# Kernel tuning notes

Measured on AMD Instinct MI355X. Metric: run time of the kernel, lower is better.

Reference implementation:

```python
import jax, jax.numpy as jnp
import numpy as np

B, D_MODEL, HIDEEN, HEAD, IMG_H, IMG_W = 16, 512, 512, 8, 32, 32
D_K = D_MODEL // HEAD
EPS = 1e-5


def setup_inputs() -> dict:
    key = jax.random.key(0)
    ks = jax.random.split(key, 9)
    s_in = 1.0 / np.sqrt(D_MODEL)
    s_h = 1.0 / np.sqrt(HIDEEN)
    return {
        "x": jax.random.normal(ks[0], (B, D_MODEL, IMG_H, IMG_W), jnp.float32),
        "Wq": jax.random.uniform(ks[1], (HIDEEN, D_MODEL), jnp.float32, -s_in, s_in),
        "bq": jax.random.uniform(ks[2], (HIDEEN,), jnp.float32, -s_in, s_in),
        "Wk": jax.random.uniform(ks[3], (HIDEEN, D_MODEL), jnp.float32, -s_in, s_in),
        "bk": jax.random.uniform(ks[4], (HIDEEN,), jnp.float32, -s_in, s_in),
        "Wv": jax.random.uniform(ks[5], (HIDEEN, D_MODEL), jnp.float32, -s_in, s_in),
        "bv": jax.random.uniform(ks[6], (HIDEEN,), jnp.float32, -s_in, s_in),
        "Wo": jax.random.uniform(ks[7], (HIDEEN, HIDEEN), jnp.float32, -s_h, s_h),
        "bo": jax.random.uniform(ks[8], (HIDEEN,), jnp.float32, -s_h, s_h),
    }


def _conv1x1(x, W, b):
    # x: [B, Cin, H, W], W: [Cout, Cin]
    return jnp.einsum("bchw,oc->bohw", x, W) + b[None, :, None, None]


def _heads(t):
    # torch: [B, C, H, W] -> view(B, -1, head, d_k) -> transpose(1, 2)
    return t.reshape(B, -1, HEAD, D_K).transpose(0, 2, 1, 3)  # [B, head, N, d_k]


def reference(x, Wq, bq, Wk, bk, Wv, bv, Wo, bo):
    q = _heads(_conv1x1(x, Wq, bq))
    k = _heads(_conv1x1(x, Wk, bk))
    v = _heads(_conv1x1(x, Wv, bv))
    scores = jnp.einsum("bhnd,bhmd->bhnm", q, k) / np.sqrt(D_K).astype(np.float32)
    attn = jax.nn.softmax(scores, axis=-1)
    out = jnp.einsum("bhnm,bhmd->bhnd", attn, v)  # [B, head, N, d_k]
    # back to image layout: [B, N, head*d_k] -> [B, hideen, H, W]
    out = out.transpose(0, 2, 1, 3).reshape(B, -1, HEAD * D_K)
    out = out.transpose(0, 2, 1).reshape(B, -1, IMG_H, IMG_W)
    out = _conv1x1(out, Wo, bo)
    # InstanceNorm2d (affine=False, biased var, eps=1e-5)
    mu = out.mean(axis=(2, 3), keepdims=True)
    var = out.var(axis=(2, 3), keepdims=True)
    out = (out - mu) / jnp.sqrt(var + EPS)
    # original applies the SAME attn_out conv a second time
    out = _conv1x1(out, Wo, bo)
    return out
```

## Files before the change

kernel.cpp:

```cpp
#include <hip/hip_runtime.h>


typedef short bf16x8_t __attribute__((ext_vector_type(8)));
typedef float f32x4_t  __attribute__((ext_vector_type(4)));

union U4 {
  uint4 u;
  bf16x8_t v;
  unsigned short us[8];
};

__device__ __forceinline__ unsigned short f2bf(float f) {
  union { float f; unsigned int u; } x; x.f = f;
  unsigned int r = x.u + 0x7fffu + ((x.u >> 16) & 1u);
  return (unsigned short)(r >> 16);
}

#define AS1 __attribute__((address_space(1)))
#define AS3 __attribute__((address_space(3)))

__device__ __forceinline__ void gload16(const unsigned short* g,
                                        unsigned short* l) {
  __builtin_amdgcn_global_load_lds((const AS1 unsigned int*)g,
                                   (AS3 unsigned int*)l, 16, 0, 0);
}

#define BATCH_STRIDE (512 * 1024)

__global__ __launch_bounds__(256) void cvtx_k(
    const float* __restrict__ x, unsigned short* __restrict__ xb)
{
  __shared__ float tile[32][33];
  const int b = blockIdx.z, c0 = blockIdx.y * 32, n0 = blockIdx.x * 32;
  const int t = threadIdx.x;
  {
    const int cl_ = t >> 3, n4 = (t & 7) * 4;
    const float4 u = *(const float4*)(x + (size_t)b * BATCH_STRIDE
                                      + (size_t)(c0 + cl_) * 1024 + n0 + n4);
    tile[cl_][n4] = u.x; tile[cl_][n4 + 1] = u.y;
    tile[cl_][n4 + 2] = u.z; tile[cl_][n4 + 3] = u.w;
  }
  __syncthreads();
  {
    const int nl = t >> 3, c4 = (t & 7) * 4;
    ushort4 o;
    o.x = f2bf(tile[c4][nl]);     o.y = f2bf(tile[c4 + 1][nl]);
    o.z = f2bf(tile[c4 + 2][nl]); o.w = f2bf(tile[c4 + 3][nl]);
    *(ushort4*)(xb + (size_t)b * BATCH_STRIDE + (size_t)(n0 + nl) * 512
                + c0 + c4) = o;
  }
}

__global__ __launch_bounds__(256) void cvtw_k(
    const float* __restrict__ s0, const float* __restrict__ s1,
    const float* __restrict__ s2, unsigned short* __restrict__ dst)
{
  const float* s = (blockIdx.y == 0) ? s0 : (blockIdx.y == 1) ? s1 : s2;
  const int i = (blockIdx.x * 256 + threadIdx.x) * 8;
  const float4 a = *(const float4*)(s + i);
  const float4 c = *(const float4*)(s + i + 4);
  U4 o;
  o.us[0] = f2bf(a.x); o.us[1] = f2bf(a.y);
  o.us[2] = f2bf(a.z); o.us[3] = f2bf(a.w);
  o.us[4] = f2bf(c.x); o.us[5] = f2bf(c.y);
  o.us[6] = f2bf(c.z); o.us[7] = f2bf(c.w);
  *(uint4*)(dst + (size_t)blockIdx.y * 262144 + i) = o.u;
}

template<int OUTF>
__device__ __forceinline__ void gemm_core(
    const unsigned short* __restrict__ Wb, const float* __restrict__ bias,
    const unsigned short* __restrict__ src, void* __restrict__ dst,
    int m0, int n0, int b, unsigned short* sA, unsigned short* sB)
{
  const int t = threadIdx.x;
  const int lane = t & 63, wv = t >> 6, qd = lane >> 4, cl = lane & 15;
  const int wm = wv >> 1, wn = wv & 1;
  const unsigned short* srcb = src + (size_t)b * BATCH_STRIDE + (size_t)n0 * 512;
  const unsigned short* wrow = Wb + (size_t)m0 * 512;

  const int lr = lane >> 2, ls = (lane & 3) * 8;
  const int r0 = wv * 32;

  f32x4_t acc[4][4];
  #pragma unroll
  for (int i = 0; i < 4; ++i)
    #pragma unroll
    for (int f = 0; f < 4; ++f) acc[i][f] = (f32x4_t){0.f, 0.f, 0.f, 0.f};

  for (int kk = 0; kk < 512; kk += 32) {
    if (kk) __syncthreads();
    gload16(wrow + (size_t)(r0 + lr) * 512 + kk + ls,      sA + r0 * 32);
    gload16(wrow + (size_t)(r0 + 16 + lr) * 512 + kk + ls, sA + (r0 + 16) * 32);
    gload16(srcb + (size_t)(r0 + lr) * 512 + kk + ls,      sB + r0 * 32);
    gload16(srcb + (size_t)(r0 + 16 + lr) * 512 + kk + ls, sB + (r0 + 16) * 32);
    __syncthreads();

    U4 af[4], bf[4];
    #pragma unroll
    for (int i = 0; i < 4; ++i) {
      af[i].u = *(const uint4*)(sA + (wm * 64 + i * 16 + cl) * 32 + qd * 8);
      bf[i].u = *(const uint4*)(sB + (wn * 64 + i * 16 + cl) * 32 + qd * 8);
    }
    #pragma unroll
    for (int i = 0; i < 4; ++i)
      #pragma unroll
      for (int f = 0; f < 4; ++f)
        acc[i][f] = __builtin_amdgcn_mfma_f32_16x16x32_bf16(
            af[i].v, bf[f].v, acc[i][f], 0, 0, 0);
  }

  #pragma unroll
  for (int i = 0; i < 4; ++i) {
    #pragma unroll
    for (int r = 0; r < 4; ++r) {
      const int o = m0 + wm * 64 + i * 16 + qd * 4 + r;
      const float bv = bias[o];
      #pragma unroll
      for (int f = 0; f < 4; ++f) {
        const int n = n0 + wn * 64 + f * 16 + cl;
        const size_t idx = (size_t)b * BATCH_STRIDE + (size_t)o * 1024 + n;
        const float val = acc[i][f][r] + bv;
        if (OUTF) ((float*)dst)[idx] = val;
        else      ((unsigned short*)dst)[idx] = f2bf(val);
      }
    }
  }
}

struct QKVArgs {
  const unsigned short* W[3];
  const float* bias[3];
  unsigned short* dst[3];
};

__global__ __launch_bounds__(256) void qkv_k(
    QKVArgs args, const unsigned short* __restrict__ xb)
{
  __shared__ __align__(16) unsigned short sA[128 * 32];
  __shared__ __align__(16) unsigned short sB[128 * 32];
  const int widx = blockIdx.y >> 2;
  const int m0 = (blockIdx.y & 3) * 128;
  gemm_core<0>(args.W[widx], args.bias[widx], xb, args.dst[widx],
               m0, blockIdx.x * 128, blockIdx.z, sA, sB);
}

template<int OUTF>
__global__ __launch_bounds__(256) void gemm_wo_k(
    const unsigned short* __restrict__ Wb, const float* __restrict__ bias,
    const unsigned short* __restrict__ src, void* __restrict__ dst)
{
  __shared__ __align__(16) unsigned short sA[128 * 32];
  __shared__ __align__(16) unsigned short sB[128 * 32];
  gemm_core<OUTF>(Wb, bias, src, dst, blockIdx.y * 128, blockIdx.x * 128,
                  blockIdx.z, sA, sB);
}

__global__ __launch_bounds__(256) void vt_k(
    const unsigned short* __restrict__ src, unsigned short* __restrict__ dst)
{
  __shared__ unsigned short tile[32][36];
  const int b = blockIdx.z, j0 = blockIdx.y * 32, p0 = blockIdx.x * 32;
  const int t = threadIdx.x;
  {
    const int pr = t >> 3, jc = (t & 7) * 4;
    *(ushort4*)&tile[pr][jc] = *(const ushort4*)(
        src + (size_t)b * BATCH_STRIDE + (size_t)(p0 + pr) * 512 + j0 + jc);
  }
  __syncthreads();
  {
    const int jr = t >> 3, pc = (t & 7) * 4;
    ushort4 o;
    o.x = tile[pc][jr];     o.y = tile[pc + 1][jr];
    o.z = tile[pc + 2][jr]; o.w = tile[pc + 3][jr];
    *(ushort4*)(dst + (size_t)b * BATCH_STRIDE + (size_t)(j0 + jr) * 1024
                + p0 + pc) = o;
  }
}

__global__ __launch_bounds__(256) void attn_k(
    const unsigned short* __restrict__ Q,
    const unsigned short* __restrict__ K,
    const unsigned short* __restrict__ Vt,
    unsigned short* __restrict__ O)
{
  __shared__ __align__(16) unsigned short sK[64 * 72];
  __shared__ __align__(16) unsigned short sV[64 * 72];
  __shared__ __align__(16) unsigned short sP[4 * 16 * 72];

  const int t = threadIdx.x;
  const int lane = t & 63, wv = t >> 6, qd = lane >> 4, cl = lane & 15;

  const int g = blockIdx.y * 16 + blockIdx.x;
  const int xcd = g & 7, rest = g >> 3;
  const int iblk = rest & 15;
  const int bh = (rest >> 4) * 8 + xcd;
  const int b = bh >> 3, h = bh & 7;
  const int i0 = iblk * 64;
  const size_t bbase = (size_t)b * BATCH_STRIDE;
  const int hoff = h * 64;

  U4 aq0, aq1;
  {
    const unsigned short* qp =
        Q + bbase + (size_t)(i0 + wv * 16 + cl) * 512 + hoff + qd * 8;
    aq0.u = *(const uint4*)qp;
    aq1.u = *(const uint4*)(qp + 32);
  }

  f32x4_t oacc[4];
  #pragma unroll
  for (int f = 0; f < 4; ++f) oacc[f] = (f32x4_t){0.f, 0.f, 0.f, 0.f};
  float rs[4] = {0.f, 0.f, 0.f, 0.f};

  for (int j0 = 0; j0 < 1024; j0 += 64) {
    __syncthreads();
    #pragma unroll
    for (int p = 0; p < 2; ++p) {
      const int row = p * 32 + (t >> 3), c8 = (t & 7) * 8;
      *(uint4*)(sK + row * 72 + c8) =
          *(const uint4*)(K + bbase + (size_t)(j0 + row) * 512 + hoff + c8);
      *(uint4*)(sV + row * 72 + c8) =
          *(const uint4*)(Vt + bbase + (size_t)(hoff + row) * 1024 + j0 + c8);
    }
    __syncthreads();

    f32x4_t s[4];
    #pragma unroll
    for (int nh = 0; nh < 4; ++nh) {
      s[nh] = (f32x4_t){0.f, 0.f, 0.f, 0.f};
      U4 bk0; bk0.u = *(const uint4*)(sK + (nh * 16 + cl) * 72 + qd * 8);
      U4 bk1; bk1.u = *(const uint4*)(sK + (nh * 16 + cl) * 72 + 32 + qd * 8);
      s[nh] = __builtin_amdgcn_mfma_f32_16x16x32_bf16(aq0.v, bk0.v, s[nh], 0, 0, 0);
      s[nh] = __builtin_amdgcn_mfma_f32_16x16x32_bf16(aq1.v, bk1.v, s[nh], 0, 0, 0);
    }

    #pragma unroll
    for (int nh = 0; nh < 4; ++nh) {
      #pragma unroll
      for (int r = 0; r < 4; ++r) {
        const float pv = __expf(s[nh][r] * 0.125f);
        sP[wv * 1152 + (qd * 4 + r) * 72 + nh * 16 + cl] = f2bf(pv);
        rs[r] += pv;
      }
    }

    __syncthreads();

    U4 pf0, pf1;
    pf0.u = *(const uint4*)(sP + wv * 1152 + cl * 72 + qd * 8);
    pf1.u = *(const uint4*)(sP + wv * 1152 + cl * 72 + 32 + qd * 8);
    #pragma unroll
    for (int f = 0; f < 4; ++f) {
      U4 vf0, vf1;
      vf0.u = *(const uint4*)(sV + (f * 16 + cl) * 72 + qd * 8);
      vf1.u = *(const uint4*)(sV + (f * 16 + cl) * 72 + 32 + qd * 8);
      oacc[f] = __builtin_amdgcn_mfma_f32_16x16x32_bf16(pf0.v, vf0.v, oacc[f], 0, 0, 0);
      oacc[f] = __builtin_amdgcn_mfma_f32_16x16x32_bf16(pf1.v, vf1.v, oacc[f], 0, 0, 0);
    }
  }

  #pragma unroll
  for (int m = 1; m < 16; m <<= 1)
    #pragma unroll
    for (int r = 0; r < 4; ++r) rs[r] += __shfl_xor(rs[r], m);

  #pragma unroll
  for (int f = 0; f < 4; ++f) {
    #pragma unroll
    for (int r = 0; r < 4; ++r) {
      const int i = i0 + wv * 16 + qd * 4 + r;
      const int j = hoff + f * 16 + cl;
      O[bbase + (size_t)i * 512 + j] = f2bf(oacc[f][r] / rs[r]);
    }
  }
}

__global__ __launch_bounds__(256) void norm_k(
    const float* __restrict__ x, unsigned short* __restrict__ y)
{
  __shared__ float tile[8][1028];
  __shared__ float shm[8], shv[8];
  const int b = blockIdx.x >> 6, c0 = (blockIdx.x & 63) * 8;
  const int t = threadIdx.x;
  const int ch = t >> 5, ln = t & 31;
  const float* xr = x + (size_t)b * BATCH_STRIDE + (size_t)(c0 + ch) * 1024;
  float s1 = 0.f, s2 = 0.f;
  #pragma unroll
  for (int j = 0; j < 8; ++j) {
    const int n = ln * 4 + j * 128;
    const float4 u = *(const float4*)(xr + n);
    tile[ch][n] = u.x; tile[ch][n + 1] = u.y;
    tile[ch][n + 2] = u.z; tile[ch][n + 3] = u.w;
    s1 += u.x + u.y + u.z + u.w;
    s2 += u.x * u.x + u.y * u.y + u.z * u.z + u.w * u.w;
  }
  #pragma unroll
  for (int m = 1; m < 32; m <<= 1) {
    s1 += __shfl_xor(s1, m);
    s2 += __shfl_xor(s2, m);
  }
  if (ln == 0) {
    const float mean = s1 * (1.f / 1024.f);
    const float var = s2 * (1.f / 1024.f) - mean * mean;
    shm[ch] = mean;
    shv[ch] = rsqrtf(var + 1e-5f);
  }
  __syncthreads();
  unsigned short* yb = y + (size_t)b * BATCH_STRIDE;
  #pragma unroll
  for (int jn = 0; jn < 4; ++jn) {
    const int n = t + jn * 256;
    U4 o;
    #pragma unroll
    for (int c = 0; c < 8; ++c)
      o.us[c] = f2bf((tile[c][n] - shm[c]) * shv[c]);
    *(uint4*)(yb + (size_t)n * 512 + c0) = o.u;
  }
}

extern "C" void kernel_launch(void* const* d_in, const int* in_sizes, int n_in,
                              void* d_out, int out_size, void* d_ws, size_t ws_size,
                              hipStream_t stream) {
  const float* x  = (const float*)d_in[0];
  const float* Wq = (const float*)d_in[1];
  const float* bq = (const float*)d_in[2];
  const float* Wk = (const float*)d_in[3];
  const float* bk = (const float*)d_in[4];
  const float* Wv = (const float*)d_in[5];
  const float* bv = (const float*)d_in[6];
  const float* Wo = (const float*)d_in[7];
  const float* bo = (const float*)d_in[8];

  const size_t BUF = (size_t)16 * BATCH_STRIDE;
  unsigned short* xb = (unsigned short*)d_ws;
  unsigned short* Qb = xb + BUF;
  unsigned short* Kb = Qb + BUF;
  unsigned short* Vb = (unsigned short*)d_out;
  unsigned short* Ob = Vb + BUF;
  unsigned short* Vt = xb;
  float*          out1f = (float*)d_ws;
  unsigned short* out1n = Kb;

  unsigned short* Wbf3 = Ob;
  unsigned short* WoA  = Vb;
  unsigned short* WoB  = xb;

  QKVArgs qa;
  qa.W[0] = Wbf3; qa.W[1] = Wbf3 + 262144; qa.W[2] = Wbf3 + 524288;
  qa.bias[0] = bq; qa.bias[1] = bk; qa.bias[2] = bv;
  qa.dst[0] = Qb; qa.dst[1] = Kb; qa.dst[2] = Vb;

  cvtx_k<<<dim3(32, 16, 16), 256, 0, stream>>>(x, xb);
  cvtw_k<<<dim3(128, 3), 256, 0, stream>>>(Wq, Wk, Wv, Wbf3);
  qkv_k<<<dim3(8, 12, 16), 256, 0, stream>>>(qa, xb);
  vt_k<<<dim3(32, 16, 16), 256, 0, stream>>>(Vb, Vt);
  cvtw_k<<<dim3(128, 1), 256, 0, stream>>>(Wo, Wo, Wo, WoA);
  attn_k<<<dim3(16, 128), 256, 0, stream>>>(Qb, Kb, Vt, Ob);
  gemm_wo_k<1><<<dim3(8, 4, 16), 256, 0, stream>>>(WoA, bo, Ob, out1f);
  norm_k<<<dim3(16 * 64), 256, 0, stream>>>(out1f, out1n);
  cvtw_k<<<dim3(128, 1), 256, 0, stream>>>(Wo, Wo, Wo, WoB);
  gemm_wo_k<1><<<dim3(8, 4, 16), 256, 0, stream>>>(WoB, bo, out1n, d_out);
}
```

Measured before the change: 268.2 us.

## Double-buffer K/V tiles with async global-to-LDS loads and XOR swizzle

```diff
diff --git a/kernel.cpp b/kernel.cpp
--- a/kernel.cpp
+++ b/kernel.cpp
@@ -184,8 +184,8 @@
     const unsigned short* __restrict__ Vt,
     unsigned short* __restrict__ O)
 {
-  __shared__ __align__(16) unsigned short sK[64 * 72];
-  __shared__ __align__(16) unsigned short sV[64 * 72];
+  __shared__ __align__(16) unsigned short sK2[2][64 * 64];
+  __shared__ __align__(16) unsigned short sV2[2][64 * 64];
   __shared__ __align__(16) unsigned short sP[4 * 16 * 72];
 
   const int t = threadIdx.x;
@@ -208,29 +208,51 @@
     aq1.u = *(const uint4*)(qp + 32);
   }
 
+  const int lrow = lane >> 3;
+  const int lchk = ((lane & 7) ^ lrow) * 8;
+  const int sw = cl & 7;
+  const int c0r = (qd ^ sw) * 8;
+  const int c1r = ((qd + 4) ^ sw) * 8;
+
   f32x4_t oacc[4];
   #pragma unroll
   for (int f = 0; f < 4; ++f) oacc[f] = (f32x4_t){0.f, 0.f, 0.f, 0.f};
   float rs[4] = {0.f, 0.f, 0.f, 0.f};
 
-  for (int j0 = 0; j0 < 1024; j0 += 64) {
-    __syncthreads();
-    #pragma unroll
-    for (int p = 0; p < 2; ++p) {
-      const int row = p * 32 + (t >> 3), c8 = (t & 7) * 8;
-      *(uint4*)(sK + row * 72 + c8) =
-          *(const uint4*)(K + bbase + (size_t)(j0 + row) * 512 + hoff + c8);
-      *(uint4*)(sV + row * 72 + c8) =
-          *(const uint4*)(Vt + bbase + (size_t)(hoff + row) * 1024 + j0 + c8);
-    }
-    __syncthreads();
+  #pragma unroll
+  for (int p = 0; p < 2; ++p) {
+    const int r = wv * 16 + p * 8;
+    gload16(K + bbase + (size_t)(r + lrow) * 512 + hoff + lchk,
+            &sK2[0][r * 64]);
+    gload16(Vt + bbase + (size_t)(hoff + r + lrow) * 1024 + lchk,
+            &sV2[0][r * 64]);
+  }
+  __syncthreads();
+
+  for (int tt = 0; tt < 16; ++tt) {
+    const unsigned short* sKb = sK2[tt & 1];
+    const unsigned short* sVb = sV2[tt & 1];
+
+    if (tt < 15) {
+      const int jn = (tt + 1) * 64;
+      unsigned short* dK = sK2[(tt + 1) & 1];
+      unsigned short* dV = sV2[(tt + 1) & 1];
+      #pragma unroll
+      for (int p = 0; p < 2; ++p) {
+        const int r = wv * 16 + p * 8;
+        gload16(K + bbase + (size_t)(jn + r + lrow) * 512 + hoff + lchk,
+                dK + r * 64);
+        gload16(Vt + bbase + (size_t)(hoff + r + lrow) * 1024 + jn + lchk,
+                dV + r * 64);
+      }
+    }
 
     f32x4_t s[4];
     #pragma unroll
     for (int nh = 0; nh < 4; ++nh) {
       s[nh] = (f32x4_t){0.f, 0.f, 0.f, 0.f};
-      U4 bk0; bk0.u = *(const uint4*)(sK + (nh * 16 + cl) * 72 + qd * 8);
-      U4 bk1; bk1.u = *(const uint4*)(sK + (nh * 16 + cl) * 72 + 32 + qd * 8);
+      U4 bk0; bk0.u = *(const uint4*)(sKb + (nh * 16 + cl) * 64 + c0r);
+      U4 bk1; bk1.u = *(const uint4*)(sKb + (nh * 16 + cl) * 64 + c1r);
       s[nh] = __builtin_amdgcn_mfma_f32_16x16x32_bf16(aq0.v, bk0.v, s[nh], 0, 0, 0);
       s[nh] = __builtin_amdgcn_mfma_f32_16x16x32_bf16(aq1.v, bk1.v, s[nh], 0, 0, 0);
     }
@@ -253,11 +275,13 @@
     #pragma unroll
     for (int f = 0; f < 4; ++f) {
       U4 vf0, vf1;
-      vf0.u = *(const uint4*)(sV + (f * 16 + cl) * 72 + qd * 8);
-      vf1.u = *(const uint4*)(sV + (f * 16 + cl) * 72 + 32 + qd * 8);
+      vf0.u = *(const uint4*)(sVb + (f * 16 + cl) * 64 + c0r);
+      vf1.u = *(const uint4*)(sVb + (f * 16 + cl) * 64 + c1r);
       oacc[f] = __builtin_amdgcn_mfma_f32_16x16x32_bf16(pf0.v, vf0.v, oacc[f], 0, 0, 0);
       oacc[f] = __builtin_amdgcn_mfma_f32_16x16x32_bf16(pf1.v, vf1.v, oacc[f], 0, 0, 0);
     }
+
+    __syncthreads();
   }
 
   #pragma unroll
```

New measurement: 272.9 us. About the same (+1.7%).
